# Kernel optimization log

Measured on AMD Instinct MI355X. Metric: run time of the kernel, lower is better.

## Reference

```python
import jax, jax.numpy as jnp
import numpy as np

B, DIM, H, W = 2, 64, 128, 128
D_STATE = 8
D_INNER = int(2.0 * DIM)          # 128
DT_RANK = int(np.ceil(DIM / 16))  # 4
CDBL = DT_RANK + 2 * D_STATE      # 20
HID = 3 * DIM                     # 192 (ffn_expansion_factor=3)
PS = 8                            # EDFFN patch size
EPS = 1e-5


def setup_inputs() -> dict:
    key = jax.random.key(0)
    ks = jax.random.split(key, 20)
    n = lambda k, s, sc=0.02: jax.random.normal(k, s, jnp.float32) * sc
    # dt bias init as in SS2D.dt_init
    rng = np.random.default_rng(0)
    dt = np.exp(rng.uniform(size=D_INNER) * (np.log(0.1) - np.log(0.001)) + np.log(0.001)).clip(min=1e-4)
    dt_b = (dt + np.log(-np.expm1(-dt))).astype(np.float32)
    A_logs = np.log(np.arange(1, D_STATE + 1, dtype=np.float32))[None, :].repeat(D_INNER, 0)
    return {
        "x": jax.random.normal(ks[0], (B, DIM, H, W), jnp.float32),
        "norm1_w": jnp.ones((DIM,), jnp.float32), "norm1_b": jnp.zeros((DIM,), jnp.float32),
        "in_proj_w": n(ks[1], (2 * D_INNER, DIM)),
        "conv2d_w": n(ks[2], (D_INNER, 1, 3, 3), 0.1), "conv2d_b": jnp.zeros((D_INNER,), jnp.float32),
        "x_proj_w": n(ks[3], (CDBL, D_INNER)),
        "x_conv_w": n(ks[4], (CDBL, 1, 7), 0.1), "x_conv_b": jnp.zeros((CDBL,), jnp.float32),
        "dt_w": n(ks[5], (D_INNER, DT_RANK), DT_RANK ** -0.5), "dt_b": jnp.asarray(dt_b),
        "A_logs": jnp.asarray(A_logs), "Ds": jnp.ones((D_INNER,), jnp.float32),
        "out_norm_w": jnp.ones((D_INNER,), jnp.float32), "out_norm_b": jnp.zeros((D_INNER,), jnp.float32),
        "out_proj_w": n(ks[6], (DIM, D_INNER)),
        "norm2_w": jnp.ones((DIM,), jnp.float32), "norm2_b": jnp.zeros((DIM,), jnp.float32),
        "pin_w": n(ks[7], (2 * HID, DIM)),
        "dw_w": n(ks[8], (2 * HID, 1, 3, 3), 0.1),
        "fft_param": jnp.ones((DIM, 1, 1, PS, PS // 2 + 1), jnp.float32),
        "pout_w": n(ks[9], (DIM, HID)),
    }


def _ln_ch(x, w, b):  # LayerNorm over channel dim of BCHW (WithBias_LayerNorm)
    mu = x.mean(1, keepdims=True)
    var = x.var(1, keepdims=True)
    return (x - mu) / jnp.sqrt(var + EPS) * w[None, :, None, None] + b[None, :, None, None]


def _dwconv2d(x, w, b=None):
    y = jax.lax.conv_general_dilated(x, w, (1, 1), [(1, 1), (1, 1)],
                                     dimension_numbers=("NCHW", "OIHW", "NCHW"),
                                     feature_group_count=x.shape[1])
    return y if b is None else y + b[None, :, None, None]


def _dwconv1d(x, w, b):
    y = jax.lax.conv_general_dilated(x, w, (1,), [(3, 3)],
                                     dimension_numbers=("NCH", "OIH", "NCH"),
                                     feature_group_count=x.shape[1])
    return y + b[None, :, None]


def _gelu(x):
    return jax.nn.gelu(x, approximate=False)


def _selective_scan(u, delta, A, Bs, Cs, Ds):
    # u, delta: [B,D,L]; A: [D,N]; Bs, Cs: [B,N,L]; Ds: [D]
    dA = jnp.exp(jnp.einsum("bdl,dn->lbdn", delta, A))          # [L,B,D,N]
    dBu = jnp.einsum("bdl,bnl->lbdn", delta * u, Bs)            # [L,B,D,N]
    Cseq = jnp.transpose(Cs, (2, 0, 1))                         # [L,B,N]

    def step(h, inp):
        dA_l, dBu_l, C_l = inp
        h = dA_l * h + dBu_l
        y = jnp.einsum("bdn,bn->bd", h, C_l)
        return h, y

    h0 = jnp.zeros(dA.shape[1:], dA.dtype)
    _, ys = jax.lax.scan(step, h0, (dA, dBu, Cseq))             # ys: [L,B,D]
    y = jnp.transpose(ys, (1, 2, 0))                            # [B,D,L]
    return y + Ds[None, :, None] * u


def _ss2d(x, in_proj_w, conv2d_w, conv2d_b, x_proj_w, x_conv_w, x_conv_b,
          dt_w, dt_b, A_logs, Ds, out_norm_w, out_norm_b, out_proj_w):
    b, c, h, w = x.shape
    xh = jnp.transpose(x, (0, 2, 3, 1))                          # [B,H,W,C]
    xz = jnp.einsum("bhwc,oc->bhwo", xh, in_proj_w)
    xi, z = jnp.split(xz, 2, axis=-1)
    xi = jnp.transpose(xi, (0, 3, 1, 2))                         # [B,Di,H,W]
    xi = _gelu(_dwconv2d(xi, conv2d_w, conv2d_b))
    L = h * w
    xs = xi.reshape(b, D_INNER, L)
    x_dbl = jnp.einsum("bdl,cd->bcl", xs, x_proj_w)
    x_dbl = _dwconv1d(x_dbl, x_conv_w, x_conv_b)
    dts, Bs, Cs = x_dbl[:, :DT_RANK], x_dbl[:, DT_RANK:DT_RANK + D_STATE], x_dbl[:, DT_RANK + D_STATE:]
    dts = jnp.einsum("brl,dr->bdl", dts, dt_w)
    delta = jax.nn.softplus(dts + dt_b[None, :, None])
    A = -jnp.exp(A_logs)
    y = _selective_scan(xs, delta, A, Bs, Cs, Ds)                # [B,Di,L]
    y = jnp.transpose(y, (0, 2, 1)).reshape(b, h, w, D_INNER)
    mu = y.mean(-1, keepdims=True)
    var = y.var(-1, keepdims=True)
    y = (y - mu) / jnp.sqrt(var + EPS) * out_norm_w + out_norm_b
    y = y * _gelu(z)
    out = jnp.einsum("bhwd,cd->bhwc", y, out_proj_w)
    return jnp.transpose(out, (0, 3, 1, 2))


def _edffn(x, pin_w, dw_w, fft_param, pout_w):
    b, c, h, w = x.shape
    y = jnp.einsum("bchw,oc->bohw", x, pin_w)                    # [B,2*HID,H,W]
    y = _dwconv2d(y, dw_w)
    x1, x2 = jnp.split(y, 2, axis=1)
    y = _gelu(x1) * x2
    y = jnp.einsum("bchw,oc->bohw", y, pout_w)                   # [B,DIM,H,W]
    # per-8x8-patch FFT filtering
    p = y.reshape(b, DIM, h // PS, PS, w // PS, PS).transpose(0, 1, 2, 4, 3, 5)
    pf = jnp.fft.rfft2(p, axes=(-2, -1)) * fft_param
    p = jnp.fft.irfft2(pf, s=(PS, PS), axes=(-2, -1))
    return p.transpose(0, 1, 2, 4, 3, 5).reshape(b, DIM, h, w)


def reference(x, norm1_w, norm1_b, in_proj_w, conv2d_w, conv2d_b, x_proj_w, x_conv_w,
              x_conv_b, dt_w, dt_b, A_logs, Ds, out_norm_w, out_norm_b, out_proj_w,
              norm2_w, norm2_b, pin_w, dw_w, fft_param, pout_w):
    # EVS forward, att=True, idx=3 (odd -> flip H,W)
    x = jnp.flip(x, axis=(-2, -1))
    x = x + _ss2d(_ln_ch(x, norm1_w, norm1_b), in_proj_w, conv2d_w, conv2d_b,
                  x_proj_w, x_conv_w, x_conv_b, dt_w, dt_b, A_logs, Ds,
                  out_norm_w, out_norm_b, out_proj_w)
    x = x + _edffn(_ln_ch(x, norm2_w, norm2_b), pin_w, dw_w, fft_param, pout_w)
    return x
```

## Files before the change

### kernel.cpp

```cpp
#include <hip/hip_runtime.h>
#include <hip/hip_bf16.h>

#define DEV __device__ __forceinline__

constexpr int BATCH = 2;
constexpr int DIM   = 64;
constexpr int HH    = 128, WW = 128;
constexpr int L     = HH * WW;
constexpr int DIN   = 128;
constexpr int DST   = 8;
constexpr int CDBL  = 20;
constexpr int HID   = 192;
constexpr int SEG   = 256;
constexpr int NSEG  = L / SEG;
constexpr int NSEGA = 256;

constexpr long OFF_XF    = 0;
constexpr long OFF_T     = OFF_XF    + (long)BATCH*DIM*L;
constexpr long OFF_XZ    = OFF_T     + (long)BATCH*DIM*L;
constexpr long OFF_XS    = OFF_XZ    + (long)BATCH*2*DIN*L;
constexpr long OFF_DBL   = OFF_XS    + (long)BATCH*DIN*L;
constexpr long OFF_DBL2  = OFF_DBL   + (long)BATCH*CDBL*L;
constexpr long OFF_DELTA = OFF_DBL2  + (long)BATCH*CDBL*L;
constexpr long OFF_Y     = OFF_DELTA + (long)BATCH*DIN*L;
constexpr long OFF_HEND  = OFF_Y     + (long)BATCH*DIN*L;
constexpr long OFF_APROD = OFF_HEND  + (long)BATCH*DIN*NSEGA*DST;
constexpr long OFF_CARRY = OFF_APROD + (long)BATCH*DIN*NSEGA*DST;
constexpr long OFF_H1    = OFF_XS;
constexpr long OFF_YFF   = OFF_H1    + (long)BATCH*2*HID*L;
constexpr long OFF_CDT   = OFF_DELTA;

DEV float gelu_f(float x) { return 0.5f * x * (1.0f + erff(x * 0.70710678118654752f)); }
DEV float softplus_f(float x) { return fmaxf(x, 0.f) + log1pf(__expf(-fabsf(x))); }

template<bool FLIPSAVE>
__global__ void ln_ch_k(const float* __restrict__ in, const float* __restrict__ w,
                        const float* __restrict__ bvec, float* __restrict__ outn,
                        float* __restrict__ src_out) {
    int l = blockIdx.x * 256 + threadIdx.x;
    int b = blockIdx.y;
    long base = (long)b * DIM * L;
    int sl = FLIPSAVE ? (L - 1 - l) : l;
    float v[DIM];
    float mu = 0.f;
    #pragma unroll
    for (int c = 0; c < DIM; c++) { v[c] = in[base + (long)c * L + sl]; mu += v[c]; }
    mu *= (1.f / DIM);
    float var = 0.f;
    #pragma unroll
    for (int c = 0; c < DIM; c++) { float d = v[c] - mu; var += d * d; }
    var *= (1.f / DIM);
    float rs = rsqrtf(var + 1e-5f);
    #pragma unroll
    for (int c = 0; c < DIM; c++) {
        long o = base + (long)c * L + l;
        if (FLIPSAVE) src_out[o] = v[c];
        outn[o] = (v[c] - mu) * rs * w[c] + bvec[c];
    }
}

template<int N, int K, int NT, int PIX, int ACT>
__global__ void gemm4(const float* __restrict__ in, long in_bs,
                      const float* __restrict__ Wm,
                      float* __restrict__ out, long out_bs,
                      const float* __restrict__ aux, long aux_bs) {
    static_assert(N % NT == 0, "NT");
    int l = (blockIdx.x * 256 + threadIdx.x) * PIX;
    int b = blockIdx.y;
    int n0 = blockIdx.z * NT;
    const float* Ap = in + (long)b * in_bs + l;
    float acc[NT][PIX];
    #pragma unroll
    for (int i = 0; i < NT; i++)
        #pragma unroll
        for (int p = 0; p < PIX; p++) acc[i][p] = 0.f;
    #pragma unroll 4
    for (int k = 0; k < K; k++) {
        float a[PIX];
        if (PIX == 4) {
            float4 a4 = *(const float4*)(Ap + (long)k * L);
            a[0] = a4.x; a[1] = a4.y; a[2] = a4.z; a[3] = a4.w;
        } else if (PIX == 2) {
            float2 a2 = *(const float2*)(Ap + (long)k * L);
            a[0] = a2.x; a[1] = a2.y;
        } else {
            a[0] = Ap[(long)k * L];
        }
        #pragma unroll
        for (int i = 0; i < NT; i++) {
            float wv = Wm[(long)(n0 + i) * K + k];
            #pragma unroll
            for (int p = 0; p < PIX; p++) acc[i][p] = fmaf(a[p], wv, acc[i][p]);
        }
    }
    #pragma unroll
    for (int i = 0; i < NT; i++) {
        long pos = (long)b * out_bs + (long)(n0 + i) * L + l;
        float r[PIX];
        #pragma unroll
        for (int p = 0; p < PIX; p++) r[p] = acc[i][p];
        if (ACT == 2) {
            const float* rp = aux + (long)b * aux_bs + (long)(n0 + i) * L + l;
            #pragma unroll
            for (int p = 0; p < PIX; p++) r[p] += rp[p];
        }
        if (PIX == 4) {
            float4 st = {r[0], r[1], r[2], r[3]};
            *(float4*)(out + pos) = st;
        } else if (PIX == 2) {
            float2 st = {r[0], r[1]};
            *(float2*)(out + pos) = st;
        } else {
            out[pos] = r[0];
        }
    }
}

__global__ void dwconv3x3_bias_gelu(const float* __restrict__ in, long in_bs,
                                    const float* __restrict__ wgt, const float* __restrict__ bias,
                                    float* __restrict__ out, long out_bs) {
    int l4 = (blockIdx.x * 256 + threadIdx.x) * 4;
    int c = blockIdx.y, b = blockIdx.z;
    int h = l4 >> 7, w = l4 & 127;
    const float* ip = in + (long)b * in_bs + (long)c * L;
    float wv[9];
    #pragma unroll
    for (int i = 0; i < 9; i++) wv[i] = wgt[c * 9 + i];
    float bz = bias[c];
    float acc[4] = {bz, bz, bz, bz};
    #pragma unroll
    for (int kh = 0; kh < 3; kh++) {
        int hh = h + kh - 1;
        if (hh < 0 || hh >= HH) continue;
        const float* row = ip + hh * WW + w;
        float4 m = *(const float4*)row;
        float e[6];
        e[0] = (w > 0) ? row[-1] : 0.f;
        e[1] = m.x; e[2] = m.y; e[3] = m.z; e[4] = m.w;
        e[5] = (w < 124) ? row[4] : 0.f;
        #pragma unroll
        for (int kw = 0; kw < 3; kw++)
            #pragma unroll
            for (int p = 0; p < 4; p++)
                acc[p] = fmaf(wv[kh * 3 + kw], e[kw + p], acc[p]);
    }
    float4 st = {gelu_f(acc[0]), gelu_f(acc[1]), gelu_f(acc[2]), gelu_f(acc[3])};
    *(float4*)(out + (long)b * out_bs + (long)c * L + l4) = st;
}

__global__ void dwconv1d7(const float* __restrict__ in, const float* __restrict__ wgt,
                          const float* __restrict__ bias, float* __restrict__ out) {
    int l4 = (blockIdx.x * 256 + threadIdx.x) * 4;
    int c = blockIdx.y, b = blockIdx.z;
    const float* ip = in + ((long)b * CDBL + c) * L;
    float wv[7];
    #pragma unroll
    for (int k = 0; k < 7; k++) wv[k] = wgt[c * 7 + k];
    float bz = bias[c];
    float e[10];
    float4 m = *(const float4*)(ip + l4);
    e[0] = (l4 >= 3) ? ip[l4 - 3] : 0.f;
    e[1] = (l4 >= 2) ? ip[l4 - 2] : 0.f;
    e[2] = (l4 >= 1) ? ip[l4 - 1] : 0.f;
    e[3] = m.x; e[4] = m.y; e[5] = m.z; e[6] = m.w;
    e[7] = (l4 + 4 < L) ? ip[l4 + 4] : 0.f;
    e[8] = (l4 + 5 < L) ? ip[l4 + 5] : 0.f;
    e[9] = (l4 + 6 < L) ? ip[l4 + 6] : 0.f;
    float acc[4] = {bz, bz, bz, bz};
    #pragma unroll
    for (int k = 0; k < 7; k++)
        #pragma unroll
        for (int p = 0; p < 4; p++)
            acc[p] = fmaf(wv[k], e[p + k], acc[p]);
    float4 st = {acc[0], acc[1], acc[2], acc[3]};
    *(float4*)(out + ((long)b * CDBL + c) * L + l4) = st;
}

__global__ void scan_p1y(const float* __restrict__ u, const float* __restrict__ dbl2,
                         const float* __restrict__ A_logs, const float* __restrict__ dtw,
                         const float* __restrict__ dtb, const float* __restrict__ Ds,
                         float* __restrict__ y0, float* __restrict__ cdt_out,
                         float* __restrict__ hend, float* __restrict__ aprod) {
    int seg = blockIdx.x, b = blockIdx.z;
    int wave = threadIdx.x >> 6, lane = threadIdx.x & 63;
    int d = blockIdx.y * 4 + wave;
    long bd = (long)b * DIN + d;
    int e0 = seg * SEG + lane * 4;
    const float* base = dbl2 + (long)b * CDBL * L + e0;
    float4 r0 = *(const float4*)(base + 0L * L);
    float4 r1 = *(const float4*)(base + 1L * L);
    float4 r2 = *(const float4*)(base + 2L * L);
    float4 r3 = *(const float4*)(base + 3L * L);
    float w0 = dtw[d * 4 + 0], w1 = dtw[d * 4 + 1], w2 = dtw[d * 4 + 2], w3 = dtw[d * 4 + 3];
    float dtbv = dtb[d];
    float dt[4];
    dt[0] = softplus_f(dtbv + w0 * r0.x + w1 * r1.x + w2 * r2.x + w3 * r3.x);
    dt[1] = softplus_f(dtbv + w0 * r0.y + w1 * r1.y + w2 * r2.y + w3 * r3.y);
    dt[2] = softplus_f(dtbv + w0 * r0.z + w1 * r1.z + w2 * r2.z + w3 * r3.z);
    dt[3] = softplus_f(dtbv + w0 * r0.w + w1 * r1.w + w2 * r2.w + w3 * r3.w);
    float c0 = dt[0], c1 = c0 + dt[1], c2 = c1 + dt[2], c3 = c2 + dt[3];
    float S = c3;
    #pragma unroll
    for (int s = 1; s < 64; s <<= 1) {
        float pv = __shfl_up(S, s, 64);
        if (lane >= s) S += pv;
    }
    float Sex = S - c3;
    float4 cd = {c0 + Sex, c1 + Sex, c2 + Sex, c3 + Sex};
    *(float4*)(cdt_out + bd * L + e0) = cd;
    float4 u4 = *(const float4*)(u + bd * L + e0);
    float du[4] = {dt[0] * u4.x, dt[1] * u4.y, dt[2] * u4.z, dt[3] * u4.w};
    float Aexp[DST];
    #pragma unroll
    for (int n = 0; n < DST; n++) Aexp[n] = -__expf(A_logs[d * DST + n]);
    float A[DST], Bb[DST];
    #pragma unroll
    for (int n = 0; n < DST; n++) {
        float an = Aexp[n];
        float4 Bn = *(const float4*)(base + (long)(4 + n) * L);
        float a0 = __expf(dt[0] * an), a1 = __expf(dt[1] * an);
        float a2 = __expf(dt[2] * an), a3 = __expf(dt[3] * an);
        float h = du[0] * Bn.x;
        h = fmaf(a1, h, du[1] * Bn.y);
        h = fmaf(a2, h, du[2] * Bn.z);
        h = fmaf(a3, h, du[3] * Bn.w);
        A[n] = a0 * a1 * a2 * a3;
        Bb[n] = h;
    }
    #pragma unroll
    for (int s = 1; s < 64; s <<= 1) {
        #pragma unroll
        for (int n = 0; n < DST; n++) {
            float pa = __shfl_up(A[n], s, 64);
            float pb = __shfl_up(Bb[n], s, 64);
            if (lane >= s) { Bb[n] = fmaf(A[n], pb, Bb[n]); A[n] *= pa; }
        }
    }
    if (lane == 63) {
        #pragma unroll
        for (int n = 0; n < DST; n++) {
            long idx = (bd * DST + n) * NSEG + seg;
            hend[idx] = Bb[n]; aprod[idx] = A[n];
        }
    }
    float Dv = Ds[d];
    float yv[4] = {Dv * u4.x, Dv * u4.y, Dv * u4.z, Dv * u4.w};
    #pragma unroll
    for (int n = 0; n < DST; n++) {
        float bE = __shfl_up(Bb[n], 1, 64);
        if (lane == 0) bE = 0.f;
        float h = bE;
        float an = Aexp[n];
        float4 Bn = *(const float4*)(base + (long)(4 + n) * L);
        float4 Cn = *(const float4*)(base + (long)(12 + n) * L);
        h = fmaf(__expf(dt[0] * an), h, du[0] * Bn.x); yv[0] = fmaf(h, Cn.x, yv[0]);
        h = fmaf(__expf(dt[1] * an), h, du[1] * Bn.y); yv[1] = fmaf(h, Cn.y, yv[1]);
        h = fmaf(__expf(dt[2] * an), h, du[2] * Bn.z); yv[2] = fmaf(h, Cn.z, yv[2]);
        h = fmaf(__expf(dt[3] * an), h, du[3] * Bn.w); yv[3] = fmaf(h, Cn.w, yv[3]);
    }
    float4 st = {yv[0], yv[1], yv[2], yv[3]};
    *(float4*)(y0 + bd * L + e0) = st;
}

__global__ void scan_p2(const float* __restrict__ hend, const float* __restrict__ aprod,
                        float* __restrict__ carryin) {
    int wave = threadIdx.x >> 6, lane = threadIdx.x & 63;
    int chain = blockIdx.x * 4 + wave;
    long idx = (long)chain * NSEG + lane;
    float a = aprod[idx], bv = hend[idx];
    #pragma unroll
    for (int s = 1; s < 64; s <<= 1) {
        float pa = __shfl_up(a, s, 64);
        float pb = __shfl_up(bv, s, 64);
        if (lane >= s) { bv = fmaf(a, pb, bv); a *= pa; }
    }
    float be = __shfl_up(bv, 1, 64);
    carryin[idx] = (lane == 0) ? 0.f : be;
}

__global__ void scan_fix(const float* __restrict__ A_logs, const float* __restrict__ dbl2,
                         const float* __restrict__ cdt, const float* __restrict__ carryin,
                         float* __restrict__ y) {
    int seg = blockIdx.x, b = blockIdx.z;
    int wave = threadIdx.x >> 6, lane = threadIdx.x & 63;
    int d = blockIdx.y * 4 + wave;
    long bd = (long)b * DIN + d;
    int e0 = seg * SEG + lane * 4;
    float4 cd = *(const float4*)(cdt + bd * L + e0);
    float4 yv = *(const float4*)(y + bd * L + e0);
    const float* cbase = dbl2 + (long)b * CDBL * L + 12L * L + e0;
    #pragma unroll
    for (int n = 0; n < DST; n++) {
        float carry = carryin[(bd * DST + n) * NSEG + seg];
        float an = -__expf(A_logs[d * DST + n]);
        float4 Cn = *(const float4*)(cbase + (long)n * L);
        yv.x = fmaf(__expf(an * cd.x) * carry, Cn.x, yv.x);
        yv.y = fmaf(__expf(an * cd.y) * carry, Cn.y, yv.y);
        yv.z = fmaf(__expf(an * cd.z) * carry, Cn.z, yv.z);
        yv.w = fmaf(__expf(an * cd.w) * carry, Cn.w, yv.w);
    }
    *(float4*)(y + bd * L + e0) = yv;
}

__global__ void out_norm_gate(const float* __restrict__ y, const float* __restrict__ xz,
                              const float* __restrict__ w, const float* __restrict__ bb,
                              float* __restrict__ out) {
    __shared__ float sS[4][64], sQ[4][64];
    int wave = threadIdx.x >> 6, lane = threadIdx.x & 63;
    int b = blockIdx.y;
    int p = (blockIdx.x * 2 + (wave >> 1)) * 64 + lane;
    int ch0 = (wave & 1) * 64;
    const float* yp = y + (long)b * DIN * L + (long)ch0 * L + p;
    float v[64];
    float s1 = 0.f, s2 = 0.f;
    #pragma unroll
    for (int c = 0; c < 64; c++) {
        v[c] = yp[(long)c * L];
        s1 += v[c];
        s2 = fmaf(v[c], v[c], s2);
    }
    sS[wave][lane] = s1; sQ[wave][lane] = s2;
    __syncthreads();
    float t1 = s1 + sS[wave ^ 1][lane];
    float t2 = s2 + sQ[wave ^ 1][lane];
    float mu = t1 * (1.f / DIN);
    float var = t2 * (1.f / DIN) - mu * mu;
    float rs = rsqrtf(var + 1e-5f);
    const float* zp = xz + (long)b * 2 * DIN * L + (long)(DIN + ch0) * L + p;
    float* op = out + (long)b * DIN * L + (long)ch0 * L + p;
    #pragma unroll
    for (int c = 0; c < 64; c++) {
        float zz = zp[(long)c * L];
        op[(long)c * L] = ((v[c] - mu) * rs * w[ch0 + c] + bb[ch0 + c]) * gelu_f(zz);
    }
}

__global__ void edffn_conv_gate(const float* __restrict__ in, const float* __restrict__ wgt,
                                float* __restrict__ out) {
    int l4 = (blockIdx.x * 256 + threadIdx.x) * 4;
    int c = blockIdx.y, b = blockIdx.z;
    int h = l4 >> 7, w = l4 & 127;
    const float* i1 = in + ((long)b * 2 * HID + c) * L;
    const float* i2 = i1 + (long)HID * L;
    float w1[9], w2[9];
    #pragma unroll
    for (int i = 0; i < 9; i++) { w1[i] = wgt[c * 9 + i]; w2[i] = wgt[(c + HID) * 9 + i]; }
    float a1[4] = {0.f, 0.f, 0.f, 0.f}, a2[4] = {0.f, 0.f, 0.f, 0.f};
    #pragma unroll
    for (int kh = 0; kh < 3; kh++) {
        int hh = h + kh - 1;
        if (hh < 0 || hh >= HH) continue;
        const float* r1 = i1 + hh * WW + w;
        const float* r2 = i2 + hh * WW + w;
        float4 m1 = *(const float4*)r1;
        float4 m2 = *(const float4*)r2;
        float e1[6], e2[6];
        e1[0] = (w > 0) ? r1[-1] : 0.f;  e2[0] = (w > 0) ? r2[-1] : 0.f;
        e1[1] = m1.x; e1[2] = m1.y; e1[3] = m1.z; e1[4] = m1.w;
        e2[1] = m2.x; e2[2] = m2.y; e2[3] = m2.z; e2[4] = m2.w;
        e1[5] = (w < 124) ? r1[4] : 0.f; e2[5] = (w < 124) ? r2[4] : 0.f;
        #pragma unroll
        for (int kw = 0; kw < 3; kw++)
            #pragma unroll
            for (int p = 0; p < 4; p++) {
                a1[p] = fmaf(w1[kh * 3 + kw], e1[kw + p], a1[p]);
                a2[p] = fmaf(w2[kh * 3 + kw], e2[kw + p], a2[p]);
            }
    }
    float4 st = {gelu_f(a1[0]) * a2[0], gelu_f(a1[1]) * a2[1],
                 gelu_f(a1[2]) * a2[2], gelu_f(a1[3]) * a2[3]};
    *(float4*)(out + ((long)b * HID + c) * L + l4) = st;
}

__global__ void patch_conv_res(const float* __restrict__ yff, const float* __restrict__ fp,
                               const float* __restrict__ res, float* __restrict__ out) {
    __shared__ float ct[8];
    __shared__ float gs[64];
    int c = blockIdx.y, b = blockIdx.z;
    const float PI4 = 0.78539816339744831f;
    if (threadIdx.x < 8) ct[threadIdx.x] = cosf(PI4 * (float)threadIdx.x);
    __syncthreads();
    if (threadIdx.x < 64) {
        int a = threadIdx.x >> 3, b2 = threadIdx.x & 7;
        float s = 0.f;
        for (int k1 = 0; k1 < 8; k1++) {
            float R = fp[c * 40 + k1 * 5 + 0] + ((b2 & 1) ? -1.f : 1.f) * fp[c * 40 + k1 * 5 + 4];
            for (int k2 = 1; k2 < 4; k2++)
                R += 2.f * fp[c * 40 + k1 * 5 + k2] * ct[(k2 * b2) & 7];
            s += ct[(k1 * a) & 7] * R;
        }
        gs[threadIdx.x] = s * (1.f / 64.f);
    }
    __syncthreads();
    int t = blockIdx.x * 256 + threadIdx.x;
    int patch = t >> 3, u = t & 7;
    int pi = patch >> 4, pj = patch & 15;
    const float* base = yff + ((long)b * DIM + c) * L + (pi * 8) * WW + pj * 8;
    float4 qa[8], qb[8];
    #pragma unroll
    for (int a = 0; a < 8; a++) {
        int r = (u - a) & 7;
        qa[a] = *(const float4*)(base + r * WW);
        qb[a] = *(const float4*)(base + r * WW + 4);
    }
    float acc[8];
    #pragma unroll
    for (int v = 0; v < 8; v++) acc[v] = 0.f;
    #pragma unroll
    for (int a = 0; a < 8; a++) {
        float q[8] = {qa[a].x, qa[a].y, qa[a].z, qa[a].w,
                      qb[a].x, qb[a].y, qb[a].z, qb[a].w};
        #pragma unroll
        for (int b3 = 0; b3 < 8; b3++) {
            float gv = gs[a * 8 + b3];
            #pragma unroll
            for (int v = 0; v < 8; v++)
                acc[v] = fmaf(gv, q[(v - b3) & 7], acc[v]);
        }
    }
    long o = ((long)b * DIM + c) * L + (pi * 8 + u) * WW + pj * 8;
    float4 r0 = *(const float4*)(res + o);
    float4 r1 = *(const float4*)(res + o + 4);
    float4 s0 = {acc[0] + r0.x, acc[1] + r0.y, acc[2] + r0.z, acc[3] + r0.w};
    float4 s1 = {acc[4] + r1.x, acc[5] + r1.y, acc[6] + r1.z, acc[7] + r1.w};
    *(float4*)(out + o) = s0;
    *(float4*)(out + o + 4) = s1;
}

extern "C" void kernel_launch(void* const* d_in, const int* in_sizes, int n_in,
                              void* d_out, int out_size, void* d_ws, size_t ws_size,
                              hipStream_t stream) {
    const float* x         = (const float*)d_in[0];
    const float* norm1_w   = (const float*)d_in[1];
    const float* norm1_b   = (const float*)d_in[2];
    const float* in_proj_w = (const float*)d_in[3];
    const float* conv2d_w  = (const float*)d_in[4];
    const float* conv2d_b  = (const float*)d_in[5];
    const float* x_proj_w  = (const float*)d_in[6];
    const float* x_conv_w  = (const float*)d_in[7];
    const float* x_conv_b  = (const float*)d_in[8];
    const float* dt_w      = (const float*)d_in[9];
    const float* dt_b      = (const float*)d_in[10];
    const float* A_logs    = (const float*)d_in[11];
    const float* Ds        = (const float*)d_in[12];
    const float* out_norm_w= (const float*)d_in[13];
    const float* out_norm_b= (const float*)d_in[14];
    const float* out_proj_w= (const float*)d_in[15];
    const float* norm2_w   = (const float*)d_in[16];
    const float* norm2_b   = (const float*)d_in[17];
    const float* pin_w     = (const float*)d_in[18];
    const float* dw_w      = (const float*)d_in[19];
    const float* fft_param = (const float*)d_in[20];
    const float* pout_w    = (const float*)d_in[21];
    float* ws  = (float*)d_ws;
    float* out = (float*)d_out;

    dim3 blk(256);
    const int GX  = L / 256;
    const int GX4 = L / (256 * 4);
    const int GX2 = L / (256 * 2);

    ln_ch_k<true><<<dim3(GX, BATCH), blk, 0, stream>>>(x, norm1_w, norm1_b, ws + OFF_T, ws + OFF_XF);
    gemm4<256, 64, 16, 4, 0><<<dim3(GX4, BATCH, 16), blk, 0, stream>>>(
        ws + OFF_T, (long)DIM * L, in_proj_w, ws + OFF_XZ, (long)2 * DIN * L, nullptr, 0);
    dwconv3x3_bias_gelu<<<dim3(GX4, DIN, BATCH), blk, 0, stream>>>(
        ws + OFF_XZ, (long)2 * DIN * L, conv2d_w, conv2d_b, ws + OFF_XS, (long)DIN * L);
    gemm4<20, 128, 5, 2, 0><<<dim3(GX2, BATCH, 4), blk, 0, stream>>>(
        ws + OFF_XS, (long)DIN * L, x_proj_w, ws + OFF_DBL, (long)CDBL * L, nullptr, 0);
    dwconv1d7<<<dim3(GX4, CDBL, BATCH), blk, 0, stream>>>(ws + OFF_DBL, x_conv_w, x_conv_b, ws + OFF_DBL2);
    scan_p1y<<<dim3(NSEG, DIN / 4, BATCH), blk, 0, stream>>>(
        ws + OFF_XS, ws + OFF_DBL2, A_logs, dt_w, dt_b, Ds,
        ws + OFF_Y, ws + OFF_CDT, ws + OFF_HEND, ws + OFF_APROD);
    scan_p2<<<dim3(BATCH * DIN * DST / 4), blk, 0, stream>>>(
        ws + OFF_HEND, ws + OFF_APROD, ws + OFF_CARRY);
    scan_fix<<<dim3(NSEG, DIN / 4, BATCH), blk, 0, stream>>>(
        A_logs, ws + OFF_DBL2, ws + OFF_CDT, ws + OFF_CARRY, ws + OFF_Y);
    out_norm_gate<<<dim3(L / 128, BATCH), blk, 0, stream>>>(ws + OFF_Y, ws + OFF_XZ,
                                                            out_norm_w, out_norm_b, ws + OFF_DELTA);
    gemm4<64, 128, 8, 4, 2><<<dim3(GX4, BATCH, 8), blk, 0, stream>>>(
        ws + OFF_DELTA, (long)DIN * L, out_proj_w, ws + OFF_XF, (long)DIM * L,
        ws + OFF_XF, (long)DIM * L);
    ln_ch_k<false><<<dim3(GX, BATCH), blk, 0, stream>>>(ws + OFF_XF, norm2_w, norm2_b,
                                                        ws + OFF_T, nullptr);
    gemm4<384, 64, 16, 4, 0><<<dim3(GX4, BATCH, 24), blk, 0, stream>>>(
        ws + OFF_T, (long)DIM * L, pin_w, ws + OFF_H1, (long)2 * HID * L, nullptr, 0);
    edffn_conv_gate<<<dim3(GX4, HID, BATCH), blk, 0, stream>>>(ws + OFF_H1, dw_w, ws + OFF_XZ);
    gemm4<64, 192, 8, 4, 0><<<dim3(GX4, BATCH, 8), blk, 0, stream>>>(
        ws + OFF_XZ, (long)HID * L, pout_w, ws + OFF_YFF, (long)DIM * L, nullptr, 0);
    patch_conv_res<<<dim3(8, DIM, BATCH), blk, 0, stream>>>(ws + OFF_YFF, fft_param,
                                                            ws + OFF_XF, out);
}
```

Baseline: 257.1 us.

## Fold channel LayerNorms into projection GEMMs via prescaled weights and row sums

```diff
diff --git a/kernel.cpp b/kernel.cpp
--- a/kernel.cpp
+++ b/kernel.cpp
@@ -29,33 +29,93 @@
 constexpr long OFF_H1    = OFF_XS;
 constexpr long OFF_YFF   = OFF_H1    + (long)BATCH*2*HID*L;
 constexpr long OFF_CDT   = OFF_DELTA;
+constexpr long OFF_WP1   = OFF_CARRY + (long)BATCH*DIN*NSEGA*DST;
+constexpr long OFF_WP2   = OFF_WP1 + 256*64 + 2*256;
 
 DEV float gelu_f(float x) { return 0.5f * x * (1.0f + erff(x * 0.70710678118654752f)); }
 DEV float softplus_f(float x) { return fmaxf(x, 0.f) + log1pf(__expf(-fabsf(x))); }
 
-template<bool FLIPSAVE>
-__global__ void ln_ch_k(const float* __restrict__ in, const float* __restrict__ w,
-                        const float* __restrict__ bvec, float* __restrict__ outn,
-                        float* __restrict__ src_out) {
-    int l = blockIdx.x * 256 + threadIdx.x;
+__global__ void wprep(const float* __restrict__ W1, const float* __restrict__ lnw1,
+                      const float* __restrict__ lnb1,
+                      const float* __restrict__ W2, const float* __restrict__ lnw2,
+                      const float* __restrict__ lnb2,
+                      float* __restrict__ wp1, float* __restrict__ wp2) {
+    int n = blockIdx.x * 256 + threadIdx.x;
+    if (n < 256) {
+        float s1 = 0.f, s2 = 0.f;
+        for (int k = 0; k < 64; k++) {
+            float wv = W1[n * 64 + k] * lnw1[k];
+            wp1[n * 64 + k] = wv;
+            s1 += wv;
+            s2 += W1[n * 64 + k] * lnb1[k];
+        }
+        wp1[256 * 64 + n] = s1;
+        wp1[256 * 64 + 256 + n] = s2;
+    }
+    if (n < 384) {
+        float s1 = 0.f, s2 = 0.f;
+        for (int k = 0; k < 64; k++) {
+            float wv = W2[n * 64 + k] * lnw2[k];
+            wp2[n * 64 + k] = wv;
+            s1 += wv;
+            s2 += W2[n * 64 + k] * lnb2[k];
+        }
+        wp2[384 * 64 + n] = s1;
+        wp2[384 * 64 + 384 + n] = s2;
+    }
+}
+
+template<int N, int NT, bool FLIP>
+__global__ void gemm_ln(const float* __restrict__ in, long in_bs,
+                        const float* __restrict__ wp,
+                        float* __restrict__ out, long out_bs) {
+    int l = (blockIdx.x * 256 + threadIdx.x) * 4;
     int b = blockIdx.y;
-    long base = (long)b * DIM * L;
-    int sl = FLIPSAVE ? (L - 1 - l) : l;
-    float v[DIM];
-    float mu = 0.f;
-    #pragma unroll
-    for (int c = 0; c < DIM; c++) { v[c] = in[base + (long)c * L + sl]; mu += v[c]; }
-    mu *= (1.f / DIM);
-    float var = 0.f;
-    #pragma unroll
-    for (int c = 0; c < DIM; c++) { float d = v[c] - mu; var += d * d; }
-    var *= (1.f / DIM);
-    float rs = rsqrtf(var + 1e-5f);
-    #pragma unroll
-    for (int c = 0; c < DIM; c++) {
-        long o = base + (long)c * L + l;
-        if (FLIPSAVE) src_out[o] = v[c];
-        outn[o] = (v[c] - mu) * rs * w[c] + bvec[c];
+    int n0 = blockIdx.z * NT;
+    const float* Ap = in + (long)b * in_bs;
+    float acc[NT][4];
+    #pragma unroll
+    for (int i = 0; i < NT; i++)
+        #pragma unroll
+        for (int p = 0; p < 4; p++) acc[i][p] = 0.f;
+    float sa[4] = {0.f, 0.f, 0.f, 0.f}, sq[4] = {0.f, 0.f, 0.f, 0.f};
+    #pragma unroll 4
+    for (int k = 0; k < 64; k++) {
+        float a[4];
+        if (FLIP) {
+            float4 a4 = *(const float4*)(Ap + (long)k * L + (L - 4 - l));
+            a[0] = a4.w; a[1] = a4.z; a[2] = a4.y; a[3] = a4.x;
+        } else {
+            float4 a4 = *(const float4*)(Ap + (long)k * L + l);
+            a[0] = a4.x; a[1] = a4.y; a[2] = a4.z; a[3] = a4.w;
+        }
+        #pragma unroll
+        for (int p = 0; p < 4; p++) { sa[p] += a[p]; sq[p] = fmaf(a[p], a[p], sq[p]); }
+        #pragma unroll
+        for (int i = 0; i < NT; i++) {
+            float wv = wp[(long)(n0 + i) * 64 + k];
+            #pragma unroll
+            for (int p = 0; p < 4; p++) acc[i][p] = fmaf(a[p], wv, acc[i][p]);
+        }
+    }
+    float rs[4], mrs[4];
+    #pragma unroll
+    for (int p = 0; p < 4; p++) {
+        float mu = sa[p] * (1.f / 64.f);
+        float var = sq[p] * (1.f / 64.f) - mu * mu;
+        rs[p] = rsqrtf(var + 1e-5f);
+        mrs[p] = -mu * rs[p];
+    }
+    #pragma unroll
+    for (int i = 0; i < NT; i++) {
+        float s1 = wp[(long)N * 64 + n0 + i];
+        float s2 = wp[(long)N * 64 + N + n0 + i];
+        float4 st;
+        st.x = fmaf(rs[0], acc[i][0], fmaf(mrs[0], s1, s2));
+        st.y = fmaf(rs[1], acc[i][1], fmaf(mrs[1], s1, s2));
+        st.z = fmaf(rs[2], acc[i][2], fmaf(mrs[2], s1, s2));
+        st.w = fmaf(rs[3], acc[i][3], fmaf(mrs[3], s1, s2));
+        *(float4*)(out + (long)b * out_bs + (long)(n0 + i) * L + l) = st;
     }
 }
 
@@ -103,6 +163,9 @@
             const float* rp = aux + (long)b * aux_bs + (long)(n0 + i) * L + l;
             #pragma unroll
             for (int p = 0; p < PIX; p++) r[p] += rp[p];
+        } else if (ACT == 3) {
+            float4 r4 = *(const float4*)(aux + (long)b * aux_bs + (long)(n0 + i) * L + (L - 4 - l));
+            r[0] += r4.w; r[1] += r4.z; r[2] += r4.y; r[3] += r4.x;
         }
         if (PIX == 4) {
             float4 st = {r[0], r[1], r[2], r[3]};
@@ -210,21 +273,19 @@
     *(float4*)(cdt_out + bd * L + e0) = cd;
     float4 u4 = *(const float4*)(u + bd * L + e0);
     float du[4] = {dt[0] * u4.x, dt[1] * u4.y, dt[2] * u4.z, dt[3] * u4.w};
-    float Aexp[DST];
-    #pragma unroll
-    for (int n = 0; n < DST; n++) Aexp[n] = -__expf(A_logs[d * DST + n]);
+    float ae[DST][4];
     float A[DST], Bb[DST];
     #pragma unroll
     for (int n = 0; n < DST; n++) {
-        float an = Aexp[n];
+        float an = -__expf(A_logs[d * DST + n]);
+        ae[n][0] = __expf(dt[0] * an); ae[n][1] = __expf(dt[1] * an);
+        ae[n][2] = __expf(dt[2] * an); ae[n][3] = __expf(dt[3] * an);
         float4 Bn = *(const float4*)(base + (long)(4 + n) * L);
-        float a0 = __expf(dt[0] * an), a1 = __expf(dt[1] * an);
-        float a2 = __expf(dt[2] * an), a3 = __expf(dt[3] * an);
         float h = du[0] * Bn.x;
-        h = fmaf(a1, h, du[1] * Bn.y);
-        h = fmaf(a2, h, du[2] * Bn.z);
-        h = fmaf(a3, h, du[3] * Bn.w);
-        A[n] = a0 * a1 * a2 * a3;
+        h = fmaf(ae[n][1], h, du[1] * Bn.y);
+        h = fmaf(ae[n][2], h, du[2] * Bn.z);
+        h = fmaf(ae[n][3], h, du[3] * Bn.w);
+        A[n] = (ae[n][0] * ae[n][1]) * (ae[n][2] * ae[n][3]);
         Bb[n] = h;
     }
     #pragma unroll
@@ -250,13 +311,12 @@
         float bE = __shfl_up(Bb[n], 1, 64);
         if (lane == 0) bE = 0.f;
         float h = bE;
-        float an = Aexp[n];
         float4 Bn = *(const float4*)(base + (long)(4 + n) * L);
         float4 Cn = *(const float4*)(base + (long)(12 + n) * L);
-        h = fmaf(__expf(dt[0] * an), h, du[0] * Bn.x); yv[0] = fmaf(h, Cn.x, yv[0]);
-        h = fmaf(__expf(dt[1] * an), h, du[1] * Bn.y); yv[1] = fmaf(h, Cn.y, yv[1]);
-        h = fmaf(__expf(dt[2] * an), h, du[2] * Bn.z); yv[2] = fmaf(h, Cn.z, yv[2]);
-        h = fmaf(__expf(dt[3] * an), h, du[3] * Bn.w); yv[3] = fmaf(h, Cn.w, yv[3]);
+        h = fmaf(ae[n][0], h, du[0] * Bn.x); yv[0] = fmaf(h, Cn.x, yv[0]);
+        h = fmaf(ae[n][1], h, du[1] * Bn.y); yv[1] = fmaf(h, Cn.y, yv[1]);
+        h = fmaf(ae[n][2], h, du[2] * Bn.z); yv[2] = fmaf(h, Cn.z, yv[2]);
+        h = fmaf(ae[n][3], h, du[3] * Bn.w); yv[3] = fmaf(h, Cn.w, yv[3]);
     }
     float4 st = {yv[0], yv[1], yv[2], yv[3]};
     *(float4*)(y0 + bd * L + e0) = st;
@@ -456,13 +516,14 @@
     float* out = (float*)d_out;
 
     dim3 blk(256);
-    const int GX  = L / 256;
     const int GX4 = L / (256 * 4);
     const int GX2 = L / (256 * 2);
 
-    ln_ch_k<true><<<dim3(GX, BATCH), blk, 0, stream>>>(x, norm1_w, norm1_b, ws + OFF_T, ws + OFF_XF);
-    gemm4<256, 64, 16, 4, 0><<<dim3(GX4, BATCH, 16), blk, 0, stream>>>(
-        ws + OFF_T, (long)DIM * L, in_proj_w, ws + OFF_XZ, (long)2 * DIN * L, nullptr, 0);
+    wprep<<<dim3(2), blk, 0, stream>>>(in_proj_w, norm1_w, norm1_b,
+                                       pin_w, norm2_w, norm2_b,
+                                       ws + OFF_WP1, ws + OFF_WP2);
+    gemm_ln<256, 16, true><<<dim3(GX4, BATCH, 16), blk, 0, stream>>>(
+        x, (long)DIM * L, ws + OFF_WP1, ws + OFF_XZ, (long)2 * DIN * L);
     dwconv3x3_bias_gelu<<<dim3(GX4, DIN, BATCH), blk, 0, stream>>>(
         ws + OFF_XZ, (long)2 * DIN * L, conv2d_w, conv2d_b, ws + OFF_XS, (long)DIN * L);
     gemm4<20, 128, 5, 2, 0><<<dim3(GX2, BATCH, 4), blk, 0, stream>>>(
@@ -477,13 +538,11 @@
         A_logs, ws + OFF_DBL2, ws + OFF_CDT, ws + OFF_CARRY, ws + OFF_Y);
     out_norm_gate<<<dim3(L / 128, BATCH), blk, 0, stream>>>(ws + OFF_Y, ws + OFF_XZ,
                                                             out_norm_w, out_norm_b, ws + OFF_DELTA);
-    gemm4<64, 128, 8, 4, 2><<<dim3(GX4, BATCH, 8), blk, 0, stream>>>(
+    gemm4<64, 128, 8, 4, 3><<<dim3(GX4, BATCH, 8), blk, 0, stream>>>(
         ws + OFF_DELTA, (long)DIN * L, out_proj_w, ws + OFF_XF, (long)DIM * L,
-        ws + OFF_XF, (long)DIM * L);
-    ln_ch_k<false><<<dim3(GX, BATCH), blk, 0, stream>>>(ws + OFF_XF, norm2_w, norm2_b,
-                                                        ws + OFF_T, nullptr);
-    gemm4<384, 64, 16, 4, 0><<<dim3(GX4, BATCH, 24), blk, 0, stream>>>(
-        ws + OFF_T, (long)DIM * L, pin_w, ws + OFF_H1, (long)2 * HID * L, nullptr, 0);
+        x, (long)DIM * L);
+    gemm_ln<384, 16, false><<<dim3(GX4, BATCH, 24), blk, 0, stream>>>(
+        ws + OFF_XF, (long)DIM * L, ws + OFF_WP2, ws + OFF_H1, (long)2 * HID * L);
     edffn_conv_gate<<<dim3(GX4, HID, BATCH), blk, 0, stream>>>(ws + OFF_H1, dw_w, ws + OFF_XZ);
     gemm4<64, 192, 8, 4, 0><<<dim3(GX4, BATCH, 8), blk, 0, stream>>>(
         ws + OFF_XZ, (long)HID * L, pout_w, ws + OFF_YFF, (long)DIM * L, nullptr, 0);
```

After: 249.0 us. 3.2% less time.
